# Kernel tuning notes

Measured on AMD Instinct MI355X. Metric: run time of the kernel, lower is better.

Reference implementation:

```python
import jax, jax.numpy as jnp
import numpy as np

B, N, D_MODEL, LAP = 64, 64, 256, 16


def setup_inputs() -> dict:
    key = jax.random.key(0)
    ks = jax.random.split(key, 8)
    adj = jax.random.randint(ks[0], (B, N, N), 0, 2, dtype=jnp.int32)
    node_feats = jax.random.normal(ks[1], (B, N, D_MODEL), dtype=jnp.float32)
    eigvec = jax.random.normal(ks[2], (B, N, LAP), dtype=jnp.float32)
    W_lap = jax.random.normal(ks[3], (LAP, D_MODEL), dtype=jnp.float32) / np.sqrt(LAP)
    W_edge = jax.random.normal(ks[4], (1 + 2 * LAP, D_MODEL), dtype=jnp.float32) / np.sqrt(1 + 2 * LAP)
    b_edge = jax.random.normal(ks[5], (D_MODEL,), dtype=jnp.float32) * 0.02
    type_embed = jax.random.normal(ks[6], (2, D_MODEL), dtype=jnp.float32)
    graph_tok = jax.random.normal(ks[7], (1, 1, D_MODEL), dtype=jnp.float32)
    return {"adj": adj, "node_feats": node_feats, "eigvec": eigvec,
            "W_lap": W_lap, "W_edge": W_edge, "b_edge": b_edge,
            "type_embed": type_embed, "graph_tok": graph_tok}


def reference(adj, node_feats, eigvec, W_lap, W_edge, b_edge, type_embed, graph_tok):
    b, n, _ = adj.shape
    d = graph_tok.shape[-1]
    # node tokens: feats + LapPE projection
    node_tok = node_feats + jnp.einsum('bnl,ld->bnd', eigvec, W_lap)
    # upper-triangular candidate edges (fixed M = n(n-1)/2, jit-friendly)
    iu, ju = jnp.triu_indices(n, k=1)               # [M]
    valid = adj[:, iu, ju] > 0                       # [B, M]
    # stable compaction: valid edges first (matches torch per-graph extraction order)
    order = jnp.argsort(~valid, axis=1, stable=True) # [B, M]
    src = iu[order]                                  # [B, M]
    dst = ju[order]
    valid_sorted = jnp.take_along_axis(valid, order, axis=1)
    Pu = jnp.take_along_axis(eigvec, src[..., None], axis=1)  # [B, M, LAP]
    Pv = jnp.take_along_axis(eigvec, dst[..., None], axis=1)
    m = src.shape[1]
    edge_in = jnp.concatenate([jnp.ones((b, m, 1), eigvec.dtype), Pu, Pv], axis=-1)
    etok = jnp.einsum('bmf,fd->bmd', edge_in, W_edge) + b_edge + type_embed[1]
    etok = jnp.where(valid_sorted[..., None], etok, 0.0)      # zeros at padding
    pad_mask_edges = ~valid_sorted                             # True = padding
    gtok = jnp.broadcast_to(graph_tok, (b, 1, d))
    seq_embeds = jnp.concatenate([gtok, node_tok, etok], axis=1)  # [B, 1+n+M, d]
    pad_mask = jnp.concatenate([jnp.zeros((b, 1 + n), bool), pad_mask_edges], axis=1)
    return seq_embeds, pad_mask
```

## Files before the change

### kernel.cpp

```cpp
#include <hip/hip_runtime.h>

#define B_ 64
#define N_ 64
#define D_ 256
#define LAP_ 16
#define M_ 2016
#define TOK_ 2081

typedef float v4f __attribute__((ext_vector_type(4)));

__device__ __forceinline__ void ij_from_m(int m, int& i, int& j) {
    float fm = (float)m;
    int gi = (int)((127.0f - sqrtf(127.0f * 127.0f - 8.0f * fm)) * 0.5f);
    if (gi < 0) gi = 0;
    if (gi > 62) gi = 62;
    while (gi > 0 && (127 * gi - gi * gi) / 2 > m) gi--;
    while (gi < 62 && (127 * (gi + 1) - (gi + 1) * (gi + 1)) / 2 <= m) gi++;
    i = gi;
    j = gi + 1 + (m - (127 * gi - gi * gi) / 2);
}

__global__ __launch_bounds__(256, 2) void prep_kernel(
    const int*   __restrict__ adj,
    const float* __restrict__ node_feats,
    const float* __restrict__ eigvec,
    const float* __restrict__ W_lap,
    const float* __restrict__ W_edge,
    const float* __restrict__ b_edge,
    const float* __restrict__ type_embed,
    const float* __restrict__ graph_tok,
    float*       __restrict__ out,
    float*       __restrict__ wsf,
    int*         __restrict__ src)
{
    __shared__ int   sAdj[N_ * N_];
    __shared__ float sEig[N_ * LAP_];
    __shared__ unsigned long long sWords[32];
    __shared__ int sPref[32];
    __shared__ int sTotal;

    const int b    = blockIdx.x;
    const int cg   = blockIdx.y;
    const int t    = threadIdx.x;
    const int wave = t >> 6, lane = t & 63;

#pragma unroll
    for (int r = 0; r < 4; r++)
        ((int4*)sAdj)[r * 256 + t] =
            ((const int4*)(adj + (size_t)b * (N_ * N_)))[r * 256 + t];
    ((float4*)sEig)[t] = ((const float4*)(eigvec + (size_t)b * N_ * LAP_))[t];

    const float* Wsel = (cg < 4) ? (W_edge + D_) : (W_edge + (1 + LAP_) * D_);
    const int colS = (cg & 3) * 64 + lane;
    float wc[LAP_], wlc[LAP_];
#pragma unroll
    for (int l = 0; l < LAP_; l++) {
        wc[l]  = Wsel[l * D_ + colS];
        wlc[l] = W_lap[l * D_ + t];
    }
    __syncthreads();

#pragma unroll
    for (int k = 0; k < 8; k++) {
        int m = k * 256 + t;
        int valid = 0;
        if (m < M_) {
            int i, j;
            ij_from_m(m, i, j);
            valid = (sAdj[i * N_ + j] > 0) ? 1 : 0;
        }
        unsigned long long blt = __ballot(valid);
        if (lane == 0) sWords[k * 4 + wave] = blt;
    }
    __syncthreads();

    if (t < 32) {
        int cnt = __popcll(sWords[t]);
        int inc = cnt;
#pragma unroll
        for (int off = 1; off < 32; off <<= 1) {
            int v = __shfl_up(inc, off);
            if (lane >= off) inc += v;
        }
        sPref[t] = inc - cnt;
        if (t == 31) sTotal = inc;
    }
    __syncthreads();

    float* Ub = wsf + 256 + (size_t)b * N_ * D_;
    float* Vb = Ub + (size_t)B_ * N_ * D_;
    float* Tb = (cg < 4) ? Ub : Vb;
#pragma unroll 2
    for (int n16 = 0; n16 < 16; n16++) {
        int n = wave * 16 + n16;
        const float* e = sEig + n * LAP_;
        float acc = 0.0f;
#pragma unroll
        for (int l = 0; l < LAP_; l++) acc += e[l] * wc[l];
        Tb[n * D_ + colS] = acc;
    }

    float* outB = out + (size_t)b * TOK_ * D_;
#pragma unroll 4
    for (int k = 0; k < 8; k++) {
        int n = cg * 8 + k;
        float a = node_feats[((size_t)b * N_ + n) * D_ + t];
        const float* e = sEig + n * LAP_;
#pragma unroll
        for (int l = 0; l < LAP_; l++) a += e[l] * wlc[l];
        outB[(size_t)(1 + n) * D_ + t] = a;
    }

    const int total = sTotal;
    float* maskb = out + (size_t)B_ * TOK_ * D_ + (size_t)b * TOK_;
    {
        int idx = t;
        if (idx < 252) {
            int m = cg * 252 + idx;
            int w = m >> 6, r = m & 63;
            unsigned long long word = sWords[w];
            int rank = sPref[w] + __popcll(word & ((1ull << r) - 1ull));
            int valid = (int)((word >> r) & 1ull);
            int p = valid ? rank : total + (m - rank);
            int i, j;
            ij_from_m(m, i, j);
            src[b * M_ + p] = i | (j << 6) | (valid << 12);
            maskb[1 + N_ + p] = valid ? 0.0f : 1.0f;
        }
    }

    if (cg == 0) {
        wsf[t] = W_edge[t] + b_edge[t] + type_embed[D_ + t];
        outB[t] = graph_tok[t];
        if (t < 1 + N_) maskb[t] = 0.0f;
    }
}

__global__ __launch_bounds__(256, 8) void edge_kernel(
    const float* __restrict__ wsf,
    const int*   __restrict__ src,
    float*       __restrict__ out)
{
    const int bid  = blockIdx.x;
    const int xcd  = bid & 7;
    const int idx  = bid >> 3;
    const int b    = ((idx & 7) << 3) | xcd;
    const int s    = idx >> 3;
    const int wave = threadIdx.x >> 6, lane = threadIdx.x & 63;

    v4f base4 = ((const v4f*)wsf)[lane];
    const float* Ub = wsf + 256 + (size_t)b * N_ * D_;
    const float* Vb = Ub + (size_t)B_ * N_ * D_;
    const int* sb = src + b * M_;
    float* outE = out + (size_t)b * TOK_ * D_ + (size_t)(1 + N_) * D_;

    const int p0 = s * 63;
    const int q15 = lane & 15;
    const int nq  = (63 - wave + 3) >> 2;
    int myinfo = (wave + 4 * q15 < 63) ? sb[p0 + wave + 4 * q15] : 0;

#pragma unroll 4
    for (int q = 0; q < nq; q++) {
        int info = __shfl(myinfo, q);
        int p = p0 + wave + 4 * q;
        v4f val = {0.0f, 0.0f, 0.0f, 0.0f};
        if (info & (1 << 12)) {
            int si = info & 63, di = (info >> 6) & 63;
            v4f u = ((const v4f*)(Ub + si * D_))[lane];
            v4f v = ((const v4f*)(Vb + di * D_))[lane];
            val = base4 + u + v;
        }
        ((v4f*)(outE + (size_t)p * D_))[lane] = val;
    }
}

extern "C" void kernel_launch(void* const* d_in, const int* in_sizes, int n_in,
                              void* d_out, int out_size, void* d_ws, size_t ws_size,
                              hipStream_t stream) {
    const int*   adj        = (const int*)d_in[0];
    const float* node_feats = (const float*)d_in[1];
    const float* eigvec     = (const float*)d_in[2];
    const float* W_lap      = (const float*)d_in[3];
    const float* W_edge     = (const float*)d_in[4];
    const float* b_edge     = (const float*)d_in[5];
    const float* type_embed = (const float*)d_in[6];
    const float* graph_tok  = (const float*)d_in[7];
    float* out = (float*)d_out;

    float* wsf = (float*)d_ws;
    int*   src = (int*)(wsf + 256 + 2 * (size_t)B_ * N_ * D_);

    prep_kernel<<<dim3(B_, 8), dim3(256), 0, stream>>>(
        adj, node_feats, eigvec, W_lap, W_edge, b_edge, type_embed, graph_tok,
        out, wsf, src);
    edge_kernel<<<dim3(2048), dim3(256), 0, stream>>>(wsf, src, out);
}
```

Baseline: 167.7 us.

## Split prep kernel into specialized role blocks for compaction, U/V and node tokens

Replaces the 8 uniform prep blocks per graph, each of which redundantly loaded the full adjacency and ran the ballot/scan, with 4 role-specialized blocks. Role 0 does the adjacency compaction and mask, roles 1 and 2 compute the U and V projections, and role 3 computes the node tokens. This removes the duplicated adjacency loads and scans, and only the compaction block pays the large shared-memory footprint. The trade-off is fewer blocks overall, with uneven per-block work that may leave the compaction block as the critical path. Launch bounds are also adjusted on both kernels.

```diff
diff --git a/kernel.cpp b/kernel.cpp
--- a/kernel.cpp
+++ b/kernel.cpp
@@ -20,7 +20,7 @@
     j = gi + 1 + (m - (127 * gi - gi * gi) / 2);
 }
 
-__global__ __launch_bounds__(256, 2) void prep_kernel(
+__global__ __launch_bounds__(256, 4) void prep_kernel(
     const int*   __restrict__ adj,
     const float* __restrict__ node_feats,
     const float* __restrict__ eigvec,
@@ -33,110 +33,115 @@
     float*       __restrict__ wsf,
     int*         __restrict__ src)
 {
-    __shared__ int   sAdj[N_ * N_];
-    __shared__ float sEig[N_ * LAP_];
-    __shared__ unsigned long long sWords[32];
-    __shared__ int sPref[32];
-    __shared__ int sTotal;
-
     const int b    = blockIdx.x;
-    const int cg   = blockIdx.y;
+    const int role = blockIdx.y;
     const int t    = threadIdx.x;
     const int wave = t >> 6, lane = t & 63;
 
-#pragma unroll
-    for (int r = 0; r < 4; r++)
-        ((int4*)sAdj)[r * 256 + t] =
-            ((const int4*)(adj + (size_t)b * (N_ * N_)))[r * 256 + t];
+    if (role == 0) {
+        __shared__ int sAdj[N_ * N_];
+        __shared__ unsigned long long sWords[32];
+        __shared__ int sPref[32];
+        __shared__ int sTotal;
+
+#pragma unroll
+        for (int r = 0; r < 4; r++)
+            ((int4*)sAdj)[r * 256 + t] =
+                ((const int4*)(adj + (size_t)b * (N_ * N_)))[r * 256 + t];
+        __syncthreads();
+
+#pragma unroll
+        for (int k = 0; k < 8; k++) {
+            int m = k * 256 + t;
+            int valid = 0;
+            if (m < M_) {
+                int i, j;
+                ij_from_m(m, i, j);
+                valid = (sAdj[i * N_ + j] > 0) ? 1 : 0;
+            }
+            unsigned long long blt = __ballot(valid);
+            if (lane == 0) sWords[k * 4 + wave] = blt;
+        }
+        __syncthreads();
+
+        if (t < 32) {
+            int cnt = __popcll(sWords[t]);
+            int inc = cnt;
+#pragma unroll
+            for (int off = 1; off < 32; off <<= 1) {
+                int v = __shfl_up(inc, off);
+                if (lane >= off) inc += v;
+            }
+            sPref[t] = inc - cnt;
+            if (t == 31) sTotal = inc;
+        }
+        __syncthreads();
+
+        const int total = sTotal;
+        float* maskb = out + (size_t)B_ * TOK_ * D_ + (size_t)b * TOK_;
+#pragma unroll
+        for (int k = 0; k < 8; k++) {
+            int m = k * 256 + t;
+            if (m < M_) {
+                int w = m >> 6, r = m & 63;
+                unsigned long long word = sWords[w];
+                int rank = sPref[w] + __popcll(word & ((1ull << r) - 1ull));
+                int valid = (int)((word >> r) & 1ull);
+                int p = valid ? rank : total + (m - rank);
+                int i, j;
+                ij_from_m(m, i, j);
+                src[b * M_ + p] = i | (j << 6) | (valid << 12);
+                maskb[1 + N_ + p] = valid ? 0.0f : 1.0f;
+            }
+        }
+        if (t < 1 + N_) maskb[t] = 0.0f;
+        return;
+    }
+
+    __shared__ float sEig[N_ * LAP_];
     ((float4*)sEig)[t] = ((const float4*)(eigvec + (size_t)b * N_ * LAP_))[t];
 
-    const float* Wsel = (cg < 4) ? (W_edge + D_) : (W_edge + (1 + LAP_) * D_);
-    const int colS = (cg & 3) * 64 + lane;
-    float wc[LAP_], wlc[LAP_];
-#pragma unroll
-    for (int l = 0; l < LAP_; l++) {
-        wc[l]  = Wsel[l * D_ + colS];
-        wlc[l] = W_lap[l * D_ + t];
-    }
+    if (role == 1 || role == 2) {
+        const float* Wsel = (role == 1) ? (W_edge + D_)
+                                        : (W_edge + (1 + LAP_) * D_);
+        float wc[LAP_];
+#pragma unroll
+        for (int l = 0; l < LAP_; l++) wc[l] = Wsel[l * D_ + t];
+        __syncthreads();
+
+        float* Tb = wsf + 256 + (size_t)b * N_ * D_
+                  + ((role == 2) ? (size_t)B_ * N_ * D_ : 0);
+#pragma unroll 4
+        for (int n = 0; n < N_; n++) {
+            const float* e = sEig + n * LAP_;
+            float acc = 0.0f;
+#pragma unroll
+            for (int l = 0; l < LAP_; l++) acc += e[l] * wc[l];
+            Tb[n * D_ + t] = acc;
+        }
+        return;
+    }
+
+    float wlc[LAP_];
+#pragma unroll
+    for (int l = 0; l < LAP_; l++) wlc[l] = W_lap[l * D_ + t];
     __syncthreads();
-
-#pragma unroll
-    for (int k = 0; k < 8; k++) {
-        int m = k * 256 + t;
-        int valid = 0;
-        if (m < M_) {
-            int i, j;
-            ij_from_m(m, i, j);
-            valid = (sAdj[i * N_ + j] > 0) ? 1 : 0;
-        }
-        unsigned long long blt = __ballot(valid);
-        if (lane == 0) sWords[k * 4 + wave] = blt;
-    }
-    __syncthreads();
-
-    if (t < 32) {
-        int cnt = __popcll(sWords[t]);
-        int inc = cnt;
-#pragma unroll
-        for (int off = 1; off < 32; off <<= 1) {
-            int v = __shfl_up(inc, off);
-            if (lane >= off) inc += v;
-        }
-        sPref[t] = inc - cnt;
-        if (t == 31) sTotal = inc;
-    }
-    __syncthreads();
-
-    float* Ub = wsf + 256 + (size_t)b * N_ * D_;
-    float* Vb = Ub + (size_t)B_ * N_ * D_;
-    float* Tb = (cg < 4) ? Ub : Vb;
-#pragma unroll 2
-    for (int n16 = 0; n16 < 16; n16++) {
-        int n = wave * 16 + n16;
-        const float* e = sEig + n * LAP_;
-        float acc = 0.0f;
-#pragma unroll
-        for (int l = 0; l < LAP_; l++) acc += e[l] * wc[l];
-        Tb[n * D_ + colS] = acc;
-    }
 
     float* outB = out + (size_t)b * TOK_ * D_;
 #pragma unroll 4
-    for (int k = 0; k < 8; k++) {
-        int n = cg * 8 + k;
+    for (int n = 0; n < N_; n++) {
         float a = node_feats[((size_t)b * N_ + n) * D_ + t];
         const float* e = sEig + n * LAP_;
 #pragma unroll
         for (int l = 0; l < LAP_; l++) a += e[l] * wlc[l];
         outB[(size_t)(1 + n) * D_ + t] = a;
     }
-
-    const int total = sTotal;
-    float* maskb = out + (size_t)B_ * TOK_ * D_ + (size_t)b * TOK_;
-    {
-        int idx = t;
-        if (idx < 252) {
-            int m = cg * 252 + idx;
-            int w = m >> 6, r = m & 63;
-            unsigned long long word = sWords[w];
-            int rank = sPref[w] + __popcll(word & ((1ull << r) - 1ull));
-            int valid = (int)((word >> r) & 1ull);
-            int p = valid ? rank : total + (m - rank);
-            int i, j;
-            ij_from_m(m, i, j);
-            src[b * M_ + p] = i | (j << 6) | (valid << 12);
-            maskb[1 + N_ + p] = valid ? 0.0f : 1.0f;
-        }
-    }
-
-    if (cg == 0) {
+    outB[t] = graph_tok[t];
+    if (b == 0)
         wsf[t] = W_edge[t] + b_edge[t] + type_embed[D_ + t];
-        outB[t] = graph_tok[t];
-        if (t < 1 + N_) maskb[t] = 0.0f;
-    }
-}
-
-__global__ __launch_bounds__(256, 8) void edge_kernel(
+}
+
+__global__ __launch_bounds__(256, 4) void edge_kernel(
     const float* __restrict__ wsf,
     const int*   __restrict__ src,
     float*       __restrict__ out)
@@ -190,7 +195,7 @@
     float* wsf = (float*)d_ws;
     int*   src = (int*)(wsf + 256 + 2 * (size_t)B_ * N_ * D_);
 
-    prep_kernel<<<dim3(B_, 8), dim3(256), 0, stream>>>(
+    prep_kernel<<<dim3(B_, 4), dim3(256), 0, stream>>>(
         adj, node_feats, eigvec, W_lap, W_edge, b_edge, type_embed, graph_tok,
         out, wsf, src);
     edge_kernel<<<dim3(2048), dim3(256), 0, stream>>>(wsf, src, out);
```

After: 175.1 us. 1.04x slower.
